# Kernel optimization log

Hardware: AMD Instinct MI355X
Metric: run time of the kernel (lower is better)

## Reference

```python
import jax, jax.numpy as jnp
import numpy as np

B, N, L, H, V, OV, MAX_STEPS = 16, 256, 4, 128, 512, 1000, 48


def setup_inputs() -> dict:
    key = jax.random.key(0)
    ks = jax.random.split(key, 20)
    s = lambda fan_in: 1.0 / np.sqrt(fan_in)
    return {
        'data': jax.random.randint(ks[0], (B, N, L), 0, V, dtype=jnp.int32),
        'true_branch_nodes': jax.random.randint(ks[1], (B, N), 0, N, dtype=jnp.int32),
        'false_branch_nodes': jax.random.randint(ks[2], (B, N), 0, N, dtype=jnp.int32),
        'start_index': jax.random.randint(ks[3], (B,), 0, N, dtype=jnp.int32),
        'exit_index': jax.random.randint(ks[4], (B,), 0, N, dtype=jnp.int32),
        'steps': jax.random.randint(ks[5], (B,), 1, MAX_STEPS + 1, dtype=jnp.int32),
        'embed_w': jax.random.uniform(ks[6], (V, H), jnp.float32, -0.1, 0.1),
        'Wi0': jax.random.normal(ks[7], (H, 4 * H), jnp.float32) * s(H),
        'Wh0': jax.random.normal(ks[8], (H, 4 * H), jnp.float32) * s(H),
        'b0': jnp.zeros((4 * H,), jnp.float32),
        'Wi1': jax.random.normal(ks[9], (H, 4 * H), jnp.float32) * s(H),
        'Wh1': jax.random.normal(ks[10], (H, 4 * H), jnp.float32) * s(H),
        'b1': jnp.zeros((4 * H,), jnp.float32),
        'branch_w': jax.random.normal(ks[11], (4 * H, 2), jnp.float32) * s(4 * H),
        'branch_b': jax.random.normal(ks[12], (2,), jnp.float32) * 1e-6,
        'out_w': jax.random.normal(ks[13], (H, OV), jnp.float32) * s(H),
        'out_b': jax.random.normal(ks[14], (OV,), jnp.float32) * 1e-6,
    }


def _lstm(c, h, x, Wi, Wh, b):
    # flax LSTMCell gate order: i, f, g, o
    z = x @ Wi + h @ Wh + b
    i, f, g, o = jnp.split(z, 4, axis=-1)
    c = jax.nn.sigmoid(f) * c + jax.nn.sigmoid(i) * jnp.tanh(g)
    h = jax.nn.sigmoid(o) * jnp.tanh(c)
    return c, h


def reference(data, true_branch_nodes, false_branch_nodes, start_index, exit_index, steps,
              embed_w, Wi0, Wh0, b0, Wi1, Wh1, b1, branch_w, branch_b, out_w, out_b):
    num_nodes = data.shape[1]

    def single_example(data_e, true_idx, false_idx, start, exit_i, n_steps):
        emb_t = jnp.swapaxes(embed_w[data_e], 0, 1)  # [L, N, H]
        hs0 = tuple(jnp.zeros((num_nodes, H), embed_w.dtype) for _ in range(4))  # (c0,h0,c1,h1)
        ip0 = jnp.zeros((num_nodes,), embed_w.dtype).at[start].set(1.0)

        def execute(hs):
            # run 2-layer stacked LSTM over each node's statement tokens (vectorized over nodes)
            def tok_step(carry, x):
                c0, h0, c1, h1 = carry
                c0, h0 = _lstm(c0, h0, x, Wi0, Wh0, b0)
                c1, h1 = _lstm(c1, h1, h0, Wi1, Wh1, b1)
                return (c0, h0, c1, h1), None
            carry, _ = jax.lax.scan(tok_step, hs, emb_t)
            return carry

        def step(carry, idx):
            hs, ip = carry
            contrib = execute(hs)
            # exit node keeps its previous hidden state
            contrib = tuple(c.at[exit_i].set(h[exit_i]) for c, h in zip(contrib, hs))
            concat = jnp.concatenate(contrib, axis=-1)  # [N, 4H]
            p = jax.nn.softmax(concat @ branch_w + branch_b, axis=-1)
            pt, pf = p[:, 0], p[:, 1]
            wt, wf = pt * ip, pf * ip
            ip_new = (jax.ops.segment_sum(wt, true_idx, num_segments=num_nodes)
                      + jax.ops.segment_sum(wf, false_idx, num_segments=num_nodes))
            denom = (ip_new + 1e-7)[:, None]
            def agg(hleaf):
                t = jax.ops.segment_sum(hleaf * wt[:, None], true_idx, num_segments=num_nodes)
                f = jax.ops.segment_sum(hleaf * wf[:, None], false_idx, num_segments=num_nodes)
                return (t + f) / denom
            hs_new = tuple(agg(hleaf) for hleaf in contrib)
            active = idx < n_steps
            hs = tuple(jnp.where(active, new, old) for new, old in zip(hs_new, hs))
            ip = jnp.where(active, ip_new, ip)
            return (hs, ip), None

        (hs, ip), _ = jax.lax.scan(step, (hs0, ip0), jnp.arange(MAX_STEPS))
        return hs[3][exit_i] @ out_w + out_b  # top-layer h at exit node -> [OV]

    return jax.vmap(single_example)(data, true_branch_nodes, false_branch_nodes,
                                    start_index, exit_index, steps)
```

## Files before the change

### kernel.cpp

```cpp
#include <hip/hip_runtime.h>

namespace {
constexpr int B = 16, N = 256, L = 4, H = 128, V = 512, OV = 1000, MAX_STEPS = 48;
constexpr int Z = 4 * H;
constexpr int BN = B * N;
constexpr int PADK = 132;
}

typedef __attribute__((ext_vector_type(8))) short short8;
typedef __attribute__((ext_vector_type(4))) float f32x4;

union F8 {
    short8 s;
    uint4 u;
    uint2 h[2];
};

__device__ __forceinline__ float sigf(float x) { return 1.0f / (1.0f + __expf(-x)); }
__device__ __forceinline__ float tanh_f(float x) { return 1.0f - 2.0f / (__expf(2.0f * x) + 1.0f); }

__device__ __forceinline__ unsigned short bf16_rne(float x) {
    unsigned u = __float_as_uint(x);
    return (unsigned short)((u + 0x7fffu + ((u >> 16) & 1u)) >> 16);
}
__device__ __forceinline__ void split2(float x, unsigned short& hi, unsigned short& lo) {
    hi = bf16_rne(x);
    const float hf = __uint_as_float(((unsigned)hi) << 16);
    lo = bf16_rne(x - hf);
}

__global__ __launch_bounds__(256) void k_init(float4* __restrict__ cur4,
                                              float* __restrict__ ip,
                                              const int* __restrict__ start) {
    const int idx = blockIdx.x * 256 + threadIdx.x;
    cur4[idx] = make_float4(0.f, 0.f, 0.f, 0.f);
    if (idx < BN) ip[idx] = ((idx & (N - 1)) == start[idx >> 8]) ? 1.0f : 0.0f;
}

__global__ __launch_bounds__(256) void k_tokz(const float* __restrict__ emb,
                                              const float* __restrict__ Wi0,
                                              const float* __restrict__ b0,
                                              float* __restrict__ tokz) {
    __shared__ float lds_a[16 * 128];
    float4* l4 = (float4*)lds_a;
    const int tid = threadIdx.x;
    const int c = tid & 127, rg = tid >> 7;
    const int row0 = blockIdx.x * 16;
    {
        const float4* a4 = (const float4*)emb;
        l4[tid] = a4[row0 * 32 + tid];
        l4[tid + 256] = a4[row0 * 32 + tid + 256];
    }
    __syncthreads();
    float acc[8][4];
    {
        float bq[4];
#pragma unroll
        for (int q = 0; q < 4; q++) bq[q] = b0[c + q * 128];
#pragma unroll
        for (int i = 0; i < 8; i++)
#pragma unroll
            for (int q = 0; q < 4; q++) acc[i][q] = bq[q];
    }
    for (int k4 = 0; k4 < 32; k4++) {
        float4 a[8];
#pragma unroll
        for (int i = 0; i < 8; i++) a[i] = l4[(rg * 8 + i) * 32 + k4];
#pragma unroll
        for (int j = 0; j < 4; j++) {
            const int k = k4 * 4 + j;
            const float* wr = Wi0 + k * Z + c;
            const float w0 = wr[0], w1 = wr[128], w2 = wr[256], w3 = wr[384];
#pragma unroll
            for (int i = 0; i < 8; i++) {
                const float av = (j == 0) ? a[i].x : (j == 1) ? a[i].y : (j == 2) ? a[i].z : a[i].w;
                acc[i][0] += av * w0;
                acc[i][1] += av * w1;
                acc[i][2] += av * w2;
                acc[i][3] += av * w3;
            }
        }
    }
#pragma unroll
    for (int i = 0; i < 8; i++) {
        const int row = row0 + rg * 8 + i;
#pragma unroll
        for (int q = 0; q < 4; q++) tokz[row * Z + c + q * 128] = acc[i][q];
    }
}

__global__ __launch_bounds__(256) void k_pack(const float* __restrict__ Wh0,
                                              const float* __restrict__ Wi1,
                                              const float* __restrict__ Wh1,
                                              unsigned short* __restrict__ WPhi,
                                              unsigned short* __restrict__ WPlo) {
    const int gid = blockIdx.x * 256 + threadIdx.x;
    const int lp = gid & 63;
    const int ks = (gid >> 6) & 3;
    const int w = (gid >> 8) & 7;
    const int q = (gid >> 11) & 3;
    const int split = (gid >> 13) & 1;
    const int mat = gid >> 14;
    const float* W = (mat == 0) ? Wh0 : (mat == 1) ? Wi1 : Wh1;
    const int g = lp >> 4, li = lp & 15;
    const int col = q * 128 + w * 16 + li;
    const int e = ((mat * 4 + q) * 8 + w) * 4 + ks;
    unsigned short* dst = (split ? WPlo : WPhi) + (size_t)e * 512 + lp * 8;
#pragma unroll
    for (int j = 0; j < 8; j++) {
        const int k = ks * 32 + ((j & 4) ? 16 : 0) + g * 4 + (j & 3);
        const float x = W[k * Z + col];
        const unsigned short hi = bf16_rne(x);
        unsigned short v = hi;
        if (split) {
            const float hf = __uint_as_float(((unsigned)hi) << 16);
            v = bf16_rne(x - hf);
        }
        dst[j] = v;
    }
}

__global__ __launch_bounds__(256) void k_csr(const int* __restrict__ tix,
                                             const int* __restrict__ fix,
                                             int* __restrict__ off,
                                             int* __restrict__ ent) {
    const int b = blockIdx.x;
    const int m = threadIdx.x;
    __shared__ int cnt[N];
    __shared__ int wsum[4];
    cnt[m] = 0;
    __syncthreads();
    const int ti = tix[b * N + m];
    const int fi = fix[b * N + m];
    atomicAdd(&cnt[ti], 1);
    atomicAdd(&cnt[fi], 1);
    __syncthreads();
    const int v = cnt[m];
    const int lane = m & 63, w = m >> 6;
    int sc = v;
#pragma unroll
    for (int o = 1; o < 64; o <<= 1) {
        const int t = __shfl_up(sc, o);
        if (lane >= o) sc += t;
    }
    if (lane == 63) wsum[w] = sc;
    __syncthreads();
    int add = 0;
    for (int i = 0; i < w; i++) add += wsum[i];
    const int base = sc - v + add;
    off[b * (N + 1) + m] = base;
    if (m == N - 1) off[b * (N + 1) + N] = base + v;
    __syncthreads();
    cnt[m] = base;
    __syncthreads();
    const int p1 = atomicAdd(&cnt[ti], 1);
    ent[b * 2 * N + p1] = (m << 1);
    const int p2 = atomicAdd(&cnt[fi], 1);
    ent[b * 2 * N + p2] = (m << 1) | 1;
}

__global__ __launch_bounds__(512) void k_scan(
    const float* __restrict__ c0c, const float* __restrict__ h0c,
    const float* __restrict__ c1c, const float* __restrict__ h1c,
    float* __restrict__ c0w, float* __restrict__ h0w,
    float* __restrict__ c1w, float* __restrict__ h1w,
    const unsigned short* __restrict__ WPhi, const unsigned short* __restrict__ WPlo,
    const float* __restrict__ b1,
    const float* __restrict__ tokz, const int* __restrict__ data,
    const float* __restrict__ bw, const float* __restrict__ bb,
    const float* __restrict__ ip, float* __restrict__ wt, float* __restrict__ wf,
    const int* __restrict__ exiti, const int* __restrict__ steps, const int s) {
    const int bx = blockIdx.x;
    const int b = bx >> 4;
    if (s >= steps[b]) return;
    const int row0 = bx * 16;
    const int tid = threadIdx.x;
    const int w = tid >> 6;
    const int l = tid & 63;
    const int g = l >> 4, li = l & 15;
    const int ch = w * 16 + li;

    __shared__ unsigned short h0hi[16 * PADK], h0lo[16 * PADK];
    __shared__ unsigned short h1hi[16 * PADK], h1lo[16 * PADK];
    __shared__ float red[16][8][2];

    float c0[4], c1[4], h0[4], h1[4];
#pragma unroll
    for (int r = 0; r < 4; r++) {
        const int off = (row0 + g * 4 + r) * H + ch;
        c0[r] = c0c[off];
        h0[r] = h0c[off];
        c1[r] = c1c[off];
        h1[r] = h1c[off];
    }
    float b1v[4];
#pragma unroll
    for (int q = 0; q < 4; q++) b1v[q] = b1[q * 128 + ch];

#pragma unroll
    for (int r = 0; r < 4; r++) {
        unsigned short hi, lo;
        split2(h0[r], hi, lo);
        h0hi[(g * 4 + r) * PADK + ch] = hi;
        h0lo[(g * 4 + r) * PADK + ch] = lo;
        split2(h1[r], hi, lo);
        h1hi[(g * 4 + r) * PADK + ch] = hi;
        h1lo[(g * 4 + r) * PADK + ch] = lo;
    }
    __syncthreads();

#pragma unroll 1
    for (int t = 0; t < L; t++) {
        f32x4 acc[4];
        {
            int tok[4];
#pragma unroll
            for (int r = 0; r < 4; r++) tok[r] = data[(row0 + g * 4 + r) * L + t];
#pragma unroll
            for (int q = 0; q < 4; q++)
#pragma unroll
                for (int r = 0; r < 4; r++) acc[q][r] = tokz[tok[r] * Z + q * 128 + ch];
        }
#pragma unroll
        for (int q = 0; q < 4; q++) {
#pragma unroll
            for (int ks = 0; ks < 4; ks++) {
                F8 ahi, alo;
                const int ab = li * PADK + ks * 32 + g * 4;
                ahi.h[0] = *(const uint2*)&h0hi[ab];
                ahi.h[1] = *(const uint2*)&h0hi[ab + 16];
                alo.h[0] = *(const uint2*)&h0lo[ab];
                alo.h[1] = *(const uint2*)&h0lo[ab + 16];
                F8 bhi, blo;
                const int e = (q * 8 + w) * 4 + ks;
                bhi.u = *(const uint4*)(WPhi + (size_t)e * 512 + l * 8);
                blo.u = *(const uint4*)(WPlo + (size_t)e * 512 + l * 8);
                acc[q] = __builtin_amdgcn_mfma_f32_16x16x32_bf16(ahi.s, bhi.s, acc[q], 0, 0, 0);
                acc[q] = __builtin_amdgcn_mfma_f32_16x16x32_bf16(ahi.s, blo.s, acc[q], 0, 0, 0);
                acc[q] = __builtin_amdgcn_mfma_f32_16x16x32_bf16(alo.s, bhi.s, acc[q], 0, 0, 0);
            }
            __builtin_amdgcn_sched_barrier(0);
        }
#pragma unroll
        for (int r = 0; r < 4; r++) {
            const float cn = sigf(acc[1][r]) * c0[r] + sigf(acc[0][r]) * tanh_f(acc[2][r]);
            c0[r] = cn;
            h0[r] = sigf(acc[3][r]) * tanh_f(cn);
        }
        __syncthreads();
#pragma unroll
        for (int r = 0; r < 4; r++) {
            unsigned short hi, lo;
            split2(h0[r], hi, lo);
            h0hi[(g * 4 + r) * PADK + ch] = hi;
            h0lo[(g * 4 + r) * PADK + ch] = lo;
        }
        __syncthreads();
#pragma unroll
        for (int q = 0; q < 4; q++) {
            const float bv = b1v[q];
            acc[q][0] = bv; acc[q][1] = bv; acc[q][2] = bv; acc[q][3] = bv;
        }
#pragma unroll
        for (int q = 0; q < 4; q++) {
#pragma unroll
            for (int ks = 0; ks < 4; ks++) {
                F8 a0hi, a0lo, a1hi, a1lo;
                const int ab = li * PADK + ks * 32 + g * 4;
                a0hi.h[0] = *(const uint2*)&h0hi[ab];
                a0hi.h[1] = *(const uint2*)&h0hi[ab + 16];
                a0lo.h[0] = *(const uint2*)&h0lo[ab];
                a0lo.h[1] = *(const uint2*)&h0lo[ab + 16];
                a1hi.h[0] = *(const uint2*)&h1hi[ab];
                a1hi.h[1] = *(const uint2*)&h1hi[ab + 16];
                a1lo.h[0] = *(const uint2*)&h1lo[ab];
                a1lo.h[1] = *(const uint2*)&h1lo[ab + 16];
                F8 b1hi, b1lo, b2hi, b2lo;
                const int e1 = ((4 + q) * 8 + w) * 4 + ks;
                const int e2 = ((8 + q) * 8 + w) * 4 + ks;
                b1hi.u = *(const uint4*)(WPhi + (size_t)e1 * 512 + l * 8);
                b1lo.u = *(const uint4*)(WPlo + (size_t)e1 * 512 + l * 8);
                b2hi.u = *(const uint4*)(WPhi + (size_t)e2 * 512 + l * 8);
                b2lo.u = *(const uint4*)(WPlo + (size_t)e2 * 512 + l * 8);
                acc[q] = __builtin_amdgcn_mfma_f32_16x16x32_bf16(a0hi.s, b1hi.s, acc[q], 0, 0, 0);
                acc[q] = __builtin_amdgcn_mfma_f32_16x16x32_bf16(a0hi.s, b1lo.s, acc[q], 0, 0, 0);
                acc[q] = __builtin_amdgcn_mfma_f32_16x16x32_bf16(a0lo.s, b1hi.s, acc[q], 0, 0, 0);
                acc[q] = __builtin_amdgcn_mfma_f32_16x16x32_bf16(a1hi.s, b2hi.s, acc[q], 0, 0, 0);
                acc[q] = __builtin_amdgcn_mfma_f32_16x16x32_bf16(a1hi.s, b2lo.s, acc[q], 0, 0, 0);
                acc[q] = __builtin_amdgcn_mfma_f32_16x16x32_bf16(a1lo.s, b2hi.s, acc[q], 0, 0, 0);
            }
            __builtin_amdgcn_sched_barrier(0);
        }
#pragma unroll
        for (int r = 0; r < 4; r++) {
            const float cn = sigf(acc[1][r]) * c1[r] + sigf(acc[0][r]) * tanh_f(acc[2][r]);
            c1[r] = cn;
            h1[r] = sigf(acc[3][r]) * tanh_f(cn);
        }
        __syncthreads();
#pragma unroll
        for (int r = 0; r < 4; r++) {
            unsigned short hi, lo;
            split2(h1[r], hi, lo);
            h1hi[(g * 4 + r) * PADK + ch] = hi;
            h1lo[(g * 4 + r) * PADK + ch] = lo;
        }
        __syncthreads();
    }

    const int ex = exiti[b];
    if ((ex >> 4) == (bx & 15)) {
        const int rl = ex & 15;
#pragma unroll
        for (int r = 0; r < 4; r++) {
            if (g * 4 + r == rl) {
                const int off = (row0 + rl) * H + ch;
                c0[r] = c0c[off];
                h0[r] = h0c[off];
                c1[r] = c1c[off];
                h1[r] = h1c[off];
            }
        }
    }
#pragma unroll
    for (int r = 0; r < 4; r++) {
        const int off = (row0 + g * 4 + r) * H + ch;
        c0w[off] = c0[r];
        h0w[off] = h0[r];
        c1w[off] = c1[r];
        h1w[off] = h1[r];
    }
    float2 bwv[4];
#pragma unroll
    for (int x = 0; x < 4; x++) bwv[x] = ((const float2*)bw)[x * 128 + ch];
    float l0p[4], l1p[4];
#pragma unroll
    for (int r = 0; r < 4; r++) {
        l0p[r] = c0[r] * bwv[0].x + h0[r] * bwv[1].x + c1[r] * bwv[2].x + h1[r] * bwv[3].x;
        l1p[r] = c0[r] * bwv[0].y + h0[r] * bwv[1].y + c1[r] * bwv[2].y + h1[r] * bwv[3].y;
    }
#pragma unroll
    for (int off = 8; off > 0; off >>= 1)
#pragma unroll
        for (int r = 0; r < 4; r++) {
            l0p[r] += __shfl_xor(l0p[r], off);
            l1p[r] += __shfl_xor(l1p[r], off);
        }
    if (li == 0)
#pragma unroll
        for (int r = 0; r < 4; r++) {
            red[g * 4 + r][w][0] = l0p[r];
            red[g * 4 + r][w][1] = l1p[r];
        }
    __syncthreads();
    if (tid < 16) {
        float l0 = bb[0], l1 = bb[1];
#pragma unroll
        for (int ww = 0; ww < 8; ww++) {
            l0 += red[tid][ww][0];
            l1 += red[tid][ww][1];
        }
        const float m = fmaxf(l0, l1);
        const float e0 = __expf(l0 - m), e1 = __expf(l1 - m);
        const float inv = 1.0f / (e0 + e1);
        const float ipv = ip[row0 + tid];
        wt[row0 + tid] = e0 * inv * ipv;
        wf[row0 + tid] = e1 * inv * ipv;
    }
}

__global__ __launch_bounds__(256) void k_agg(
    const float* __restrict__ c0w, const float* __restrict__ h0w,
    const float* __restrict__ c1w, const float* __restrict__ h1w,
    float* __restrict__ c0c, float* __restrict__ h0c,
    float* __restrict__ c1c, float* __restrict__ h1c,
    const int* __restrict__ off, const int* __restrict__ ent,
    const float* __restrict__ wt, const float* __restrict__ wf,
    float* __restrict__ ip, const int* __restrict__ steps, const int s) {
    const int row00 = blockIdx.x * 4;
    const int b = row00 >> 8;
    if (s >= steps[b]) return;
    const int tid = threadIdx.x;
    const int lane = tid & 63;
    const int n = (row00 & (N - 1)) + (tid >> 6);
    const int rowb = b * N;
    const int beg = off[b * (N + 1) + n];
    const int end = off[b * (N + 1) + n + 1];
    float a00 = 0, a01 = 0, a10 = 0, a11 = 0, a20 = 0, a21 = 0, a30 = 0, a31 = 0;
    float ipacc = 0.f;
    for (int e = beg; e < end; e++) {
        const int pe = ent[b * 2 * N + e];
        const int m = pe >> 1;
        const float wgt = (pe & 1) ? wf[rowb + m] : wt[rowb + m];
        ipacc += wgt;
        const int rb = (rowb + m) * H;
        a00 += c0w[rb + lane] * wgt;
        a01 += c0w[rb + lane + 64] * wgt;
        a10 += h0w[rb + lane] * wgt;
        a11 += h0w[rb + lane + 64] * wgt;
        a20 += c1w[rb + lane] * wgt;
        a21 += c1w[rb + lane + 64] * wgt;
        a30 += h1w[rb + lane] * wgt;
        a31 += h1w[rb + lane + 64] * wgt;
    }
    const float dn = 1.0f / (ipacc + 1e-7f);
    const int ob = (rowb + n) * H;
    c0c[ob + lane] = a00 * dn;
    c0c[ob + lane + 64] = a01 * dn;
    h0c[ob + lane] = a10 * dn;
    h0c[ob + lane + 64] = a11 * dn;
    c1c[ob + lane] = a20 * dn;
    c1c[ob + lane + 64] = a21 * dn;
    h1c[ob + lane] = a30 * dn;
    h1c[ob + lane + 64] = a31 * dn;
    if (lane == 0) ip[rowb + n] = ipacc;
}

__global__ __launch_bounds__(256) void k_out(const float* __restrict__ h1c,
                                             const float* __restrict__ ow,
                                             const float* __restrict__ ob,
                                             const int* __restrict__ exiti,
                                             float* __restrict__ out) {
    const int b = blockIdx.x;
    __shared__ float h[H];
    const int tid = threadIdx.x;
    if (tid < H) h[tid] = h1c[(b * N + exiti[b]) * H + tid];
    __syncthreads();
    for (int v = tid; v < OV; v += 256) {
        float acc = ob[v];
        for (int d = 0; d < H; d++) acc += h[d] * ow[d * OV + v];
        out[b * OV + v] = acc;
    }
}

extern "C" void kernel_launch(void* const* d_in, const int* in_sizes, int n_in,
                              void* d_out, int out_size, void* d_ws, size_t ws_size,
                              hipStream_t stream) {
    (void)in_sizes; (void)n_in; (void)out_size;
    const int* data = (const int*)d_in[0];
    const int* tix = (const int*)d_in[1];
    const int* fix = (const int*)d_in[2];
    const int* start = (const int*)d_in[3];
    const int* exiti = (const int*)d_in[4];
    const int* steps = (const int*)d_in[5];
    const float* emb = (const float*)d_in[6];
    const float* Wi0 = (const float*)d_in[7];
    const float* Wh0 = (const float*)d_in[8];
    const float* b0 = (const float*)d_in[9];
    const float* Wi1 = (const float*)d_in[10];
    const float* Wh1 = (const float*)d_in[11];
    const float* b1 = (const float*)d_in[12];
    const float* bw = (const float*)d_in[13];
    const float* bb = (const float*)d_in[14];
    const float* ow = (const float*)d_in[15];
    const float* obias = (const float*)d_in[16];
    float* out = (float*)d_out;

    const size_t SB = (size_t)BN * H;
    float* ws = (float*)d_ws;
    float* c0c = ws;
    float* h0c = ws + 1 * SB;
    float* c1c = ws + 2 * SB;
    float* h1c = ws + 3 * SB;
    float* c0w = ws + 4 * SB;
    float* h0w = ws + 5 * SB;
    float* c1w = ws + 6 * SB;
    float* h1w = ws + 7 * SB;
    float* tokz = ws + 8 * SB;
    float* ip = tokz + (size_t)V * Z;
    float* wt = ip + BN;
    float* wf = wt + BN;
    unsigned short* WPhi = (unsigned short*)(wf + BN);
    unsigned short* WPlo = WPhi + 3 * 65536;
    int* csr_off = (int*)(WPlo + 3 * 65536);
    int* csr_ent = csr_off + B * (N + 1);
    const size_t need = (8 * SB + (size_t)V * Z + 3 * (size_t)BN) * sizeof(float) +
                        2 * 3 * 65536 * sizeof(unsigned short) +
                        (B * (N + 1) + B * 2 * N) * sizeof(int);
    if (ws_size < need) return;

    k_init<<<(4 * SB / 4) / 256, 256, 0, stream>>>((float4*)ws, ip, start);
    k_tokz<<<V / 16, 256, 0, stream>>>(emb, Wi0, b0, tokz);
    k_pack<<<192, 256, 0, stream>>>(Wh0, Wi1, Wh1, WPhi, WPlo);
    k_csr<<<B, 256, 0, stream>>>(tix, fix, csr_off, csr_ent);

    for (int s = 0; s < MAX_STEPS; s++) {
        k_scan<<<BN / 16, 512, 0, stream>>>(c0c, h0c, c1c, h1c, c0w, h0w, c1w, h1w,
                                            WPhi, WPlo, b1, tokz, data, bw, bb,
                                            ip, wt, wf, exiti, steps, s);
        k_agg<<<BN / 4, 256, 0, stream>>>(c0w, h0w, c1w, h1w, c0c, h0c, c1c, h1c,
                                          csr_off, csr_ent, wt, wf, ip, steps, s);
    }
    k_out<<<B, 256, 0, stream>>>(h1c, ow, obias, exiti, out);
}
```

Measured before the change: 4.659 ms.

## Halve k_scan block to 4 waves, each computing two 16-column MFMA tiles

Shrinks the k_scan block from 8 to 4 wavefronts. Each wave now handles two 16-channel column tiles, so it reuses the LDS-loaded A fragments (h hi/lo) across twice as many MFMAs and issues half as many LDS reads per output. The cost is doubled per-thread register state (c/h/acc arrays) and fewer waves per block to hide weight-load latency. launch_bounds(256,1) is set to allow the larger register footprint.

```diff
diff --git a/kernel.cpp b/kernel.cpp
--- a/kernel.cpp
+++ b/kernel.cpp
@@ -159,7 +159,7 @@
     ent[b * 2 * N + p2] = (m << 1) | 1;
 }
 
-__global__ __launch_bounds__(512) void k_scan(
+__global__ __launch_bounds__(256, 1) void k_scan(
     const float* __restrict__ c0c, const float* __restrict__ h0c,
     const float* __restrict__ c1c, const float* __restrict__ h1c,
     float* __restrict__ c0w, float* __restrict__ h0w,
@@ -178,40 +178,52 @@
     const int w = tid >> 6;
     const int l = tid & 63;
     const int g = l >> 4, li = l & 15;
-    const int ch = w * 16 + li;
+    const int ch0 = w * 32 + li;
+    const int ch1 = w * 32 + 16 + li;
 
     __shared__ unsigned short h0hi[16 * PADK], h0lo[16 * PADK];
     __shared__ unsigned short h1hi[16 * PADK], h1lo[16 * PADK];
-    __shared__ float red[16][8][2];
-
-    float c0[4], c1[4], h0[4], h1[4];
-#pragma unroll
-    for (int r = 0; r < 4; r++) {
-        const int off = (row0 + g * 4 + r) * H + ch;
-        c0[r] = c0c[off];
-        h0[r] = h0c[off];
-        c1[r] = c1c[off];
-        h1[r] = h1c[off];
-    }
-    float b1v[4];
-#pragma unroll
-    for (int q = 0; q < 4; q++) b1v[q] = b1[q * 128 + ch];
-
-#pragma unroll
-    for (int r = 0; r < 4; r++) {
-        unsigned short hi, lo;
-        split2(h0[r], hi, lo);
-        h0hi[(g * 4 + r) * PADK + ch] = hi;
-        h0lo[(g * 4 + r) * PADK + ch] = lo;
-        split2(h1[r], hi, lo);
-        h1hi[(g * 4 + r) * PADK + ch] = hi;
-        h1lo[(g * 4 + r) * PADK + ch] = lo;
+    __shared__ float red[16][4][2];
+
+    float c0[2][4], c1[2][4], h0[2][4], h1[2][4];
+#pragma unroll
+    for (int w2 = 0; w2 < 2; w2++) {
+        const int ch = w2 ? ch1 : ch0;
+#pragma unroll
+        for (int r = 0; r < 4; r++) {
+            const int off = (row0 + g * 4 + r) * H + ch;
+            c0[w2][r] = c0c[off];
+            h0[w2][r] = h0c[off];
+            c1[w2][r] = c1c[off];
+            h1[w2][r] = h1c[off];
+        }
+    }
+    float b1v[4][2];
+#pragma unroll
+    for (int q = 0; q < 4; q++) {
+        b1v[q][0] = b1[q * 128 + ch0];
+        b1v[q][1] = b1[q * 128 + ch1];
+    }
+
+#pragma unroll
+    for (int w2 = 0; w2 < 2; w2++) {
+        const int ch = w2 ? ch1 : ch0;
+#pragma unroll
+        for (int r = 0; r < 4; r++) {
+            unsigned short hi, lo;
+            split2(h0[w2][r], hi, lo);
+            h0hi[(g * 4 + r) * PADK + ch] = hi;
+            h0lo[(g * 4 + r) * PADK + ch] = lo;
+            split2(h1[w2][r], hi, lo);
+            h1hi[(g * 4 + r) * PADK + ch] = hi;
+            h1lo[(g * 4 + r) * PADK + ch] = lo;
+        }
     }
     __syncthreads();
 
 #pragma unroll 1
     for (int t = 0; t < L; t++) {
-        f32x4 acc[4];
+        f32x4 acc[4][2];
         {
             int tok[4];
 #pragma unroll
@@ -219,7 +231,10 @@
 #pragma unroll
             for (int q = 0; q < 4; q++)
 #pragma unroll
-                for (int r = 0; r < 4; r++) acc[q][r] = tokz[tok[r] * Z + q * 128 + ch];
+                for (int r = 0; r < 4; r++) {
+                    acc[q][0][r] = tokz[tok[r] * Z + q * 128 + ch0];
+                    acc[q][1][r] = tokz[tok[r] * Z + q * 128 + ch1];
+                }
         }
 #pragma unroll
         for (int q = 0; q < 4; q++) {
@@ -231,36 +246,47 @@
                 ahi.h[1] = *(const uint2*)&h0hi[ab + 16];
                 alo.h[0] = *(const uint2*)&h0lo[ab];
                 alo.h[1] = *(const uint2*)&h0lo[ab + 16];
-                F8 bhi, blo;
-                const int e = (q * 8 + w) * 4 + ks;
-                bhi.u = *(const uint4*)(WPhi + (size_t)e * 512 + l * 8);
-                blo.u = *(const uint4*)(WPlo + (size_t)e * 512 + l * 8);
-                acc[q] = __builtin_amdgcn_mfma_f32_16x16x32_bf16(ahi.s, bhi.s, acc[q], 0, 0, 0);
-                acc[q] = __builtin_amdgcn_mfma_f32_16x16x32_bf16(ahi.s, blo.s, acc[q], 0, 0, 0);
-                acc[q] = __builtin_amdgcn_mfma_f32_16x16x32_bf16(alo.s, bhi.s, acc[q], 0, 0, 0);
+#pragma unroll
+                for (int w2 = 0; w2 < 2; w2++) {
+                    F8 bhi, blo;
+                    const int e = (q * 8 + 2 * w + w2) * 4 + ks;
+                    bhi.u = *(const uint4*)(WPhi + (size_t)e * 512 + l * 8);
+                    blo.u = *(const uint4*)(WPlo + (size_t)e * 512 + l * 8);
+                    acc[q][w2] = __builtin_amdgcn_mfma_f32_16x16x32_bf16(ahi.s, bhi.s, acc[q][w2], 0, 0, 0);
+                    acc[q][w2] = __builtin_amdgcn_mfma_f32_16x16x32_bf16(ahi.s, blo.s, acc[q][w2], 0, 0, 0);
+                    acc[q][w2] = __builtin_amdgcn_mfma_f32_16x16x32_bf16(alo.s, bhi.s, acc[q][w2], 0, 0, 0);
+                }
             }
             __builtin_amdgcn_sched_barrier(0);
         }
 #pragma unroll
-        for (int r = 0; r < 4; r++) {
-            const float cn = sigf(acc[1][r]) * c0[r] + sigf(acc[0][r]) * tanh_f(acc[2][r]);
-            c0[r] = cn;
-            h0[r] = sigf(acc[3][r]) * tanh_f(cn);
-        }
+        for (int w2 = 0; w2 < 2; w2++)
+#pragma unroll
+            for (int r = 0; r < 4; r++) {
+                const float cn = sigf(acc[1][w2][r]) * c0[w2][r] + sigf(acc[0][w2][r]) * tanh_f(acc[2][w2][r]);
+                c0[w2][r] = cn;
+                h0[w2][r] = sigf(acc[3][w2][r]) * tanh_f(cn);
+            }
         __syncthreads();
 #pragma unroll
-        for (int r = 0; r < 4; r++) {
-            unsigned short hi, lo;
-            split2(h0[r], hi, lo);
-            h0hi[(g * 4 + r) * PADK + ch] = hi;
-            h0lo[(g * 4 + r) * PADK + ch] = lo;
+        for (int w2 = 0; w2 < 2; w2++) {
+            const int ch = w2 ? ch1 : ch0;
+#pragma unroll
+            for (int r = 0; r < 4; r++) {
+                unsigned short hi, lo;
+                split2(h0[w2][r], hi, lo);
+                h0hi[(g * 4 + r) * PADK + ch] = hi;
+                h0lo[(g * 4 + r) * PADK + ch] = lo;
+            }
         }
         __syncthreads();
 #pragma unroll
-        for (int q = 0; q < 4; q++) {
-            const float bv = b1v[q];
-            acc[q][0] = bv; acc[q][1] = bv; acc[q][2] = bv; acc[q][3] = bv;
-        }
+        for (int q = 0; q < 4; q++)
+#pragma unroll
+            for (int w2 = 0; w2 < 2; w2++) {
+                const float bv = b1v[q][w2];
+                acc[q][w2][0] = bv; acc[q][w2][1] = bv; acc[q][w2][2] = bv; acc[q][w2][3] = bv;
+            }
 #pragma unroll
         for (int q = 0; q < 4; q++) {
 #pragma unroll
@@ -275,35 +301,44 @@
                 a1hi.h[1] = *(const uint2*)&h1hi[ab + 16];
                 a1lo.h[0] = *(const uint2*)&h1lo[ab];
                 a1lo.h[1] = *(const uint2*)&h1lo[ab + 16];
-                F8 b1hi, b1lo, b2hi, b2lo;
-                const int e1 = ((4 + q) * 8 + w) * 4 + ks;
-                const int e2 = ((8 + q) * 8 + w) * 4 + ks;
-                b1hi.u = *(const uint4*)(WPhi + (size_t)e1 * 512 + l * 8);
-                b1lo.u = *(const uint4*)(WPlo + (size_t)e1 * 512 + l * 8);
-                b2hi.u = *(const uint4*)(WPhi + (size_t)e2 * 512 + l * 8);
-                b2lo.u = *(const uint4*)(WPlo + (size_t)e2 * 512 + l * 8);
-                acc[q] = __builtin_amdgcn_mfma_f32_16x16x32_bf16(a0hi.s, b1hi.s, acc[q], 0, 0, 0);
-                acc[q] = __builtin_amdgcn_mfma_f32_16x16x32_bf16(a0hi.s, b1lo.s, acc[q], 0, 0, 0);
-                acc[q] = __builtin_amdgcn_mfma_f32_16x16x32_bf16(a0lo.s, b1hi.s, acc[q], 0, 0, 0);
-                acc[q] = __builtin_amdgcn_mfma_f32_16x16x32_bf16(a1hi.s, b2hi.s, acc[q], 0, 0, 0);
-                acc[q] = __builtin_amdgcn_mfma_f32_16x16x32_bf16(a1hi.s, b2lo.s, acc[q], 0, 0, 0);
-                acc[q] = __builtin_amdgcn_mfma_f32_16x16x32_bf16(a1lo.s, b2hi.s, acc[q], 0, 0, 0);
+#pragma unroll
+                for (int w2 = 0; w2 < 2; w2++) {
+                    F8 b1hi, b1lo, b2hi, b2lo;
+                    const int e1 = ((4 + q) * 8 + 2 * w + w2) * 4 + ks;
+                    const int e2 = ((8 + q) * 8 + 2 * w + w2) * 4 + ks;
+                    b1hi.u = *(const uint4*)(WPhi + (size_t)e1 * 512 + l * 8);
+                    b1lo.u = *(const uint4*)(WPlo + (size_t)e1 * 512 + l * 8);
+                    b2hi.u = *(const uint4*)(WPhi + (size_t)e2 * 512 + l * 8);
+                    b2lo.u = *(const uint4*)(WPlo + (size_t)e2 * 512 + l * 8);
+                    acc[q][w2] = __builtin_amdgcn_mfma_f32_16x16x32_bf16(a0hi.s, b1hi.s, acc[q][w2], 0, 0, 0);
+                    acc[q][w2] = __builtin_amdgcn_mfma_f32_16x16x32_bf16(a0hi.s, b1lo.s, acc[q][w2], 0, 0, 0);
+                    acc[q][w2] = __builtin_amdgcn_mfma_f32_16x16x32_bf16(a0lo.s, b1hi.s, acc[q][w2], 0, 0, 0);
+                    acc[q][w2] = __builtin_amdgcn_mfma_f32_16x16x32_bf16(a1hi.s, b2hi.s, acc[q][w2], 0, 0, 0);
+                    acc[q][w2] = __builtin_amdgcn_mfma_f32_16x16x32_bf16(a1hi.s, b2lo.s, acc[q][w2], 0, 0, 0);
+                    acc[q][w2] = __builtin_amdgcn_mfma_f32_16x16x32_bf16(a1lo.s, b2hi.s, acc[q][w2], 0, 0, 0);
+                }
             }
             __builtin_amdgcn_sched_barrier(0);
         }
 #pragma unroll
-        for (int r = 0; r < 4; r++) {
-            const float cn = sigf(acc[1][r]) * c1[r] + sigf(acc[0][r]) * tanh_f(acc[2][r]);
-            c1[r] = cn;
-            h1[r] = sigf(acc[3][r]) * tanh_f(cn);
-        }
+        for (int w2 = 0; w2 < 2; w2++)
+#pragma unroll
+            for (int r = 0; r < 4; r++) {
+                const float cn = sigf(acc[1][w2][r]) * c1[w2][r] + sigf(acc[0][w2][r]) * tanh_f(acc[2][w2][r]);
+                c1[w2][r] = cn;
+                h1[w2][r] = sigf(acc[3][w2][r]) * tanh_f(cn);
+            }
         __syncthreads();
 #pragma unroll
-        for (int r = 0; r < 4; r++) {
-            unsigned short hi, lo;
-            split2(h1[r], hi, lo);
-            h1hi[(g * 4 + r) * PADK + ch] = hi;
-            h1lo[(g * 4 + r) * PADK + ch] = lo;
+        for (int w2 = 0; w2 < 2; w2++) {
+            const int ch = w2 ? ch1 : ch0;
+#pragma unroll
+            for (int r = 0; r < 4; r++) {
+                unsigned short hi, lo;
+                split2(h1[w2][r], hi, lo);
+                h1hi[(g * 4 + r) * PADK + ch] = hi;
+                h1lo[(g * 4 + r) * PADK + ch] = lo;
+            }
         }
         __syncthreads();
     }
@@ -314,30 +349,47 @@
 #pragma unroll
         for (int r = 0; r < 4; r++) {
             if (g * 4 + r == rl) {
-                const int off = (row0 + rl) * H + ch;
-                c0[r] = c0c[off];
-                h0[r] = h0c[off];
-                c1[r] = c1c[off];
-                h1[r] = h1c[off];
-            }
-        }
-    }
+#pragma unroll
+                for (int w2 = 0; w2 < 2; w2++) {
+                    const int off = (row0 + rl) * H + (w2 ? ch1 : ch0);
+                    c0[w2][r] = c0c[off];
+                    h0[w2][r] = h0c[off];
+                    c1[w2][r] = c1c[off];
+                    h1[w2][r] = h1c[off];
+                }
+            }
+        }
+    }
+#pragma unroll
+    for (int w2 = 0; w2 < 2; w2++) {
+        const int ch = w2 ? ch1 : ch0;
+#pragma unroll
+        for (int r = 0; r < 4; r++) {
+            const int off = (row0 + g * 4 + r) * H + ch;
+            c0w[off] = c0[w2][r];
+            h0w[off] = h0[w2][r];
+            c1w[off] = c1[w2][r];
+            h1w[off] = h1[w2][r];
+        }
+    }
+    float2 bwv[4][2];
+#pragma unroll
+    for (int x = 0; x < 4; x++) {
+        bwv[x][0] = ((const float2*)bw)[x * 128 + ch0];
+        bwv[x][1] = ((const float2*)bw)[x * 128 + ch1];
+    }
+    float l0p[4], l1p[4];
 #pragma unroll
     for (int r = 0; r < 4; r++) {
-        const int off = (row0 + g * 4 + r) * H + ch;
-        c0w[off] = c0[r];
-        h0w[off] = h0[r];
-        c1w[off] = c1[r];
-        h1w[off] = h1[r];
-    }
-    float2 bwv[4];
-#pragma unroll
-    for (int x = 0; x < 4; x++) bwv[x] = ((const float2*)bw)[x * 128 + ch];
-    float l0p[4], l1p[4];
-#pragma unroll
-    for (int r = 0; r < 4; r++) {
-        l0p[r] = c0[r] * bwv[0].x + h0[r] * bwv[1].x + c1[r] * bwv[2].x + h1[r] * bwv[3].x;
-        l1p[r] = c0[r] * bwv[0].y + h0[r] * bwv[1].y + c1[r] * bwv[2].y + h1[r] * bwv[3].y;
+        l0p[r] = 0.f;
+        l1p[r] = 0.f;
+#pragma unroll
+        for (int w2 = 0; w2 < 2; w2++) {
+            l0p[r] += c0[w2][r] * bwv[0][w2].x + h0[w2][r] * bwv[1][w2].x +
+                      c1[w2][r] * bwv[2][w2].x + h1[w2][r] * bwv[3][w2].x;
+            l1p[r] += c0[w2][r] * bwv[0][w2].y + h0[w2][r] * bwv[1][w2].y +
+                      c1[w2][r] * bwv[2][w2].y + h1[w2][r] * bwv[3][w2].y;
+        }
     }
 #pragma unroll
     for (int off = 8; off > 0; off >>= 1)
@@ -356,7 +408,7 @@
     if (tid < 16) {
         float l0 = bb[0], l1 = bb[1];
 #pragma unroll
-        for (int ww = 0; ww < 8; ww++) {
+        for (int ww = 0; ww < 4; ww++) {
             l0 += red[tid][ww][0];
             l1 += red[tid][ww][1];
         }
@@ -485,7 +537,7 @@
     k_csr<<<B, 256, 0, stream>>>(tix, fix, csr_off, csr_ent);
 
     for (int s = 0; s < MAX_STEPS; s++) {
-        k_scan<<<BN / 16, 512, 0, stream>>>(c0c, h0c, c1c, h1c, c0w, h0w, c1w, h1w,
+        k_scan<<<BN / 16, 256, 0, stream>>>(c0c, h0c, c1c, h1c, c0w, h0w, c1w, h1w,
                                             WPhi, WPlo, b1, tokz, data, bw, bb,
                                             ip, wt, wf, exiti, steps, s);
         k_agg<<<BN / 4, 256, 0, stream>>>(c0w, h0w, c1w, h1w, c0c, h0c, c1c, h1c,
```

Measured after the change: 5.817 ms. +24.9%, slower.
